# Optimization experiments

Hardware: AMD Instinct MI355X
Metric: run time of the kernel (lower is better)

## Reference

```python
import jax, jax.numpy as jnp
import numpy as np

B = 2048   # batch
C = 64     # EEG channels (num_eegch)
T = 125    # time samples -> pool5 -> 25 -> (p=5, 5)
H = 8      # num_heads
L = 6      # num_layers
D = 16     # num_projected_features
QK = 8     # qkv_len
P = 5      # tokens before cls
EPS = 1e-5


def setup_inputs() -> dict:
    key = jax.random.key(0)
    ks = iter(jax.random.split(key, 64))

    def nrm(shape, s=0.05):
        return jax.random.normal(next(ks), shape, jnp.float32) * s

    return {
        "x": jax.random.normal(next(ks), (B, 1, C, T), jnp.float32),
        "conv_t_w": nrm((8, 1, 1, 63)),
        "conv_t_b": nrm((8,)),
        "bn1_g": 1.0 + nrm((8,)),
        "bn1_b": nrm((8,)),
        "bn1_m": nrm((8,)),
        "bn1_v": 1.0 + 0.1 * jax.random.uniform(next(ks), (8,), jnp.float32),
        "conv_s_w": nrm((16, 1, C, 1)),
        "conv_s_b": nrm((16,)),
        "bn2_g": 1.0 + nrm((16,)),
        "bn2_b": nrm((16,)),
        "bn2_m": nrm((16,)),
        "bn2_v": 1.0 + 0.1 * jax.random.uniform(next(ks), (16,), jnp.float32),
        "proj_w": nrm((D, 16 * 5)),
        "proj_b": nrm((D,)),
        "cls_token": nrm((1, 1, D), 1.0),
        "pe": nrm((1, P + 1, D), 1.0),
        "qkv_w": nrm((L, 3 * H * QK, D)),
        "qkv_b": nrm((L, 3 * H * QK)),
        "out_w": nrm((L, D, H * QK)),
        "out_b": nrm((L, D)),
        "ln1_g": jnp.ones((L, D), jnp.float32),
        "ln1_b": jnp.zeros((L, D), jnp.float32),
        "ln2_g": jnp.ones((L, D), jnp.float32),
        "ln2_b": jnp.zeros((L, D), jnp.float32),
        "mlp_w1": nrm((L, 2 * D, D)),
        "mlp_b1": nrm((L, 2 * D)),
        "mlp_w2": nrm((L, D, 2 * D)),
        "mlp_b2": nrm((L, D)),
        "head_ln_g": jnp.ones((D,), jnp.float32),
        "head_ln_b": jnp.zeros((D,), jnp.float32),
        "head_w": nrm((2, D)),
        "head_b": nrm((2,)),
    }


def _bn(z, g, b, m, v):
    s = (g * jax.lax.rsqrt(v + EPS))[None, :, None, None]
    return (z - m[None, :, None, None]) * s + b[None, :, None, None]


def _ln(z, g, b):
    m = z.mean(-1, keepdims=True)
    var = jnp.mean((z - m) ** 2, -1, keepdims=True)
    return (z - m) * jax.lax.rsqrt(var + EPS) * g + b


def _forward(x, conv_t_w, conv_t_b, bn1_g, bn1_b, bn1_m, bn1_v,
             conv_s_w, conv_s_b, bn2_g, bn2_b, bn2_m, bn2_v,
             proj_w, proj_b, cls_token, pe,
             qkv_w, qkv_b, out_w, out_b, ln1_g, ln1_b, ln2_g, ln2_b,
             mlp_w1, mlp_b1, mlp_w2, mlp_b2,
             head_ln_g, head_ln_b, head_w, head_b):
    b = x.shape[0]
    dn = ('NCHW', 'OIHW', 'NCHW')
    # temporal conv, 'same' padding on width (kernel 63 -> pad 31/31)
    y = jax.lax.conv_general_dilated(x, conv_t_w, (1, 1), [(0, 0), (31, 31)], dimension_numbers=dn)
    y = _bn(y + conv_t_b[None, :, None, None], bn1_g, bn1_b, bn1_m, bn1_v)
    # grouped spatial conv collapses the EEG-channel axis
    y = jax.lax.conv_general_dilated(y, conv_s_w, (1, 1), 'VALID', dimension_numbers=dn, feature_group_count=8)
    y = _bn(y + conv_s_b[None, :, None, None], bn2_g, bn2_b, bn2_m, bn2_v)
    y = jax.nn.elu(y)                              # (b,16,1,125)
    y = y.reshape(b, 16, 1, T // 5, 5).mean(-1)    # avg_pool2d (1,5) -> (b,16,1,25)
    # dropout: identity at inference
    y = y.reshape(b, 16, 1, P, 5)
    y = jnp.swapaxes(y, 3, 4)
    tok = jnp.swapaxes(y.reshape(b, 16 * 5, P), 1, 2)   # (b,5,80)
    tok = tok @ proj_w.T + proj_b                       # (b,5,16)
    z = jnp.concatenate([jnp.broadcast_to(cls_token, (b, 1, D)), tok], axis=1) + pe  # (b,6,16)
    scale = QK ** -0.5
    for i in range(L):
        h1 = _ln(z, ln1_g[i], ln1_b[i])
        qkv = h1 @ qkv_w[i].T + qkv_b[i]                # (b,6,3*H*QK)
        q, k, v = jnp.split(qkv, 3, axis=-1)
        q = q.reshape(b, P + 1, H, QK).transpose(0, 2, 1, 3)
        k = k.reshape(b, P + 1, H, QK).transpose(0, 2, 1, 3)
        v = v.reshape(b, P + 1, H, QK).transpose(0, 2, 1, 3)
        att = jax.nn.softmax(jnp.einsum('bhsd,bhtd->bhst', q, k) * scale, axis=-1)
        o = jnp.einsum('bhst,bhtd->bhsd', att, v).transpose(0, 2, 1, 3).reshape(b, P + 1, H * QK)
        z = o @ out_w[i].T + out_b[i] + z
        h2 = _ln(z, ln2_g[i], ln2_b[i])
        m = jax.nn.gelu(h2 @ mlp_w1[i].T + mlp_b1[i], approximate=False) @ mlp_w2[i].T + mlp_b2[i]
        z = m + z
    cls = _ln(z[:, 0, :], head_ln_g, head_ln_b)
    return jax.nn.softmax(cls @ head_w.T + head_b, axis=-1)


def reference(x, conv_t_w, conv_t_b, bn1_g, bn1_b, bn1_m, bn1_v,
              conv_s_w, conv_s_b, bn2_g, bn2_b, bn2_m, bn2_v,
              proj_w, proj_b, cls_token, pe,
              qkv_w, qkv_b, out_w, out_b, ln1_g, ln1_b, ln2_g, ln2_b,
              mlp_w1, mlp_b1, mlp_w2, mlp_b2,
              head_ln_g, head_ln_b, head_w, head_b):
    return _forward(x, conv_t_w, conv_t_b, bn1_g, bn1_b, bn1_m, bn1_v,
                    conv_s_w, conv_s_b, bn2_g, bn2_b, bn2_m, bn2_v,
                    proj_w, proj_b, cls_token, pe,
                    qkv_w, qkv_b, out_w, out_b, ln1_g, ln1_b, ln2_g, ln2_b,
                    mlp_w1, mlp_b1, mlp_w2, mlp_b2,
                    head_ln_g, head_ln_b, head_w, head_b)
```

## Files before the change

kernel.cpp:

```cpp
#include <hip/hip_runtime.h>

#define WAVE_SYNC() do { asm volatile("" ::: "memory"); \
                         __builtin_amdgcn_wave_barrier(); \
                         asm volatile("" ::: "memory"); } while (0)

typedef _Float16 h2 __attribute__((ext_vector_type(2)));
typedef _Float16 h4 __attribute__((ext_vector_type(4)));
typedef _Float16 h8 __attribute__((ext_vector_type(8)));

__device__ __forceinline__ float fdot2(h2 a, h2 b, float c) {
#if defined(__has_builtin)
#if __has_builtin(__builtin_amdgcn_fdot2)
    return __builtin_amdgcn_fdot2(a, b, c, false);
#else
    return (float)a[0]*(float)b[0] + (float)a[1]*(float)b[1] + c;
#endif
#else
    return (float)a[0]*(float)b[0] + (float)a[1]*(float)b[1] + c;
#endif
}

__device__ __forceinline__ float dot8h(h8 a, h8 b, float c) {
    float s = c;
    #pragma unroll
    for (int i = 0; i < 4; ++i) {
        h2 x = {a[2*i], a[2*i+1]};
        h2 y = {b[2*i], b[2*i+1]};
        s = fdot2(x, y, s);
    }
    return s;
}

__device__ __forceinline__ float dot16h(h8 a0, h8 a1, h8 b0, h8 b1, float c) {
    return dot8h(a1, b1, dot8h(a0, b0, c));
}

__device__ __forceinline__ float ln_norm16(float z, float g, float bb) {
    float s = z, q = z * z;
    #pragma unroll
    for (int off = 8; off >= 1; off >>= 1) {
        s += __shfl_xor(s, off, 16);
        q += __shfl_xor(q, off, 16);
    }
    float mean = s * 0.0625f;
    float var  = q * 0.0625f - mean * mean;
    return (z - mean) * rsqrtf(var + 1e-5f) * g + bb;
}

__device__ __forceinline__ float gelu_exact(float a) {
    float xa = fabsf(a) * 0.70710678118654752f;
    float tt = 1.f / (1.f + 0.3275911f * xa);
    float poly = tt * (0.254829592f + tt * (-0.284496736f + tt * (1.421413741f
               + tt * (-1.453152027f + tt * 1.061405429f))));
    float erfv = 1.f - poly * __expf(-xa * xa);
    erfv = a >= 0.f ? erfv : -erfv;
    return 0.5f * a * (1.f + erfv);
}


#define F_XSTR 204
#define F_PL   4000
#define TOKF   4704
#define FUSED_TOTF 4784

#define WQKVH 0
#define WOUTH 4608
#define WM1H  5760
#define WM2H  6528
#define BQKVF 3584
#define BOUTF 3776
#define BM1F  3792
#define BM2F  3824
#define LN1GF 3840
#define LN1BF 3856
#define LN2GF 3872
#define LN2BF 3888
#define SCR0  7808
#define SH1H  0
#define SQKVH 144
#define SMHSH 1344

extern "C" __global__ __launch_bounds__(128, 2)
void eegnet_fused(
    const float* __restrict__ x,
    const float* __restrict__ conv_t_w, const float* __restrict__ conv_t_b,
    const float* __restrict__ bn1_g, const float* __restrict__ bn1_b,
    const float* __restrict__ bn1_m, const float* __restrict__ bn1_v,
    const float* __restrict__ conv_s_w, const float* __restrict__ conv_s_b,
    const float* __restrict__ bn2_g, const float* __restrict__ bn2_b,
    const float* __restrict__ bn2_m, const float* __restrict__ bn2_v,
    const float* __restrict__ proj_w, const float* __restrict__ proj_b,
    const float* __restrict__ cls_token, const float* __restrict__ pe,
    const float* __restrict__ qkv_w, const float* __restrict__ qkv_b,
    const float* __restrict__ out_w, const float* __restrict__ out_b,
    const float* __restrict__ ln1_g, const float* __restrict__ ln1_b,
    const float* __restrict__ ln2_g, const float* __restrict__ ln2_b,
    const float* __restrict__ mlp_w1, const float* __restrict__ mlp_b1,
    const float* __restrict__ mlp_w2, const float* __restrict__ mlp_b2,
    const float* __restrict__ head_ln_g, const float* __restrict__ head_ln_b,
    const float* __restrict__ head_w, const float* __restrict__ head_b,
    float* __restrict__ out)
{
    __shared__ __align__(16) float sm[FUSED_TOTF];
    _Float16* smh = reinterpret_cast<_Float16*>(sm);
    _Float16* xr  = reinterpret_cast<_Float16*>(sm);

    const int tid = threadIdx.x;
    const int b   = blockIdx.x;

    {
        const float4* xb4 = reinterpret_cast<const float4*>(x + (size_t)b * 8000);
        #pragma unroll
        for (int k = 0; k < 16; ++k) {
            int g = min(tid + k * 128, 1999);
            float4 v = xb4[g];
            h4 hv = {(_Float16)v.x, (_Float16)v.y, (_Float16)v.z, (_Float16)v.w};
            *reinterpret_cast<h4*>(&xr[4 * g]) = hv;
        }
    }
    __syncthreads();

    float acc[16];
    #pragma unroll
    for (int o = 0; o < 16; ++o) acc[o] = 0.f;
    {
        const int t = min(tid, 124);
        #pragma unroll 8
        for (int c = 0; c < 64; ++c) {
            float xv = (float)xr[c * 125 + t];
            #pragma unroll
            for (int o = 0; o < 16; ++o)
                acc[o] += conv_s_w[o * 64 + c] * xv;
        }
    }
    __syncthreads();

    for (int i = tid; i < 16 * 79; i += 128) {
        int row = i / 79, k = i - row * 79;
        int off = (k < 32) ? k : (k + 125);
        sm[row * F_XSTR + off] = 0.f;
    }
    if (tid < 125) {
        #pragma unroll
        for (int o = 0; o < 16; ++o)
            sm[o * F_XSTR + 32 + tid] = acc[o];
    }
    __syncthreads();

    const int oo = tid & 15, qg8 = tid >> 4, gg = oo >> 1;
    {
        float sa, cc;
        {
            float s1 = bn1_g[gg] * rsqrtf(bn1_v[gg] + 1e-5f);
            float b1 = (conv_t_b[gg] - bn1_m[gg]) * s1 + bn1_b[gg];
            float s2 = bn2_g[oo] * rsqrtf(bn2_v[oo] + 1e-5f);
            float ssum = 0.f;
            const float4* csw = reinterpret_cast<const float4*>(conv_s_w + oo * 64);
            #pragma unroll
            for (int i = 0; i < 16; ++i) {
                float4 v = csw[i];
                ssum += v.x + v.y + v.z + v.w;
            }
            sa = s1 * s2;
            cc = (b1 * ssum + conv_s_b[oo] - bn2_m[oo]) * s2 + bn2_b[oo];
        }
        float wt[63];
        #pragma unroll
        for (int k = 0; k < 63; ++k) wt[k] = conv_t_w[gg * 63 + k];

        #pragma unroll 2
        for (int jj = 0; jj < 4; ++jj) {
            int j  = qg8 * 4 + jj;
            int jc = min(j, 24);
            int base = oo * F_XSTR + 5 * jc + 1;
            float acc5[5] = {0.f, 0.f, 0.f, 0.f, 0.f};
            #pragma unroll
            for (int m = 0; m < 67; ++m) {
                float xv = sm[base + m];
                #pragma unroll
                for (int u = 0; u < 5; ++u)
                    if (u <= m && m - u <= 62) acc5[u] += wt[m - u] * xv;
            }
            float psum = 0.f;
            #pragma unroll
            for (int u = 0; u < 5; ++u) {
                float v = acc5[u] * sa + cc;
                psum += (v > 0.f) ? v : (__expf(v) - 1.f);
            }
            if (j == jc) sm[F_PL + oo * 28 + j] = psum * 0.2f;
        }
    }
    __syncthreads();

    if (tid < 80) {
        int p = tid >> 4, dd = tid & 15;
        float acc3 = proj_b[dd];
        const float4* wp = reinterpret_cast<const float4*>(proj_w + dd * 80);
        #pragma unroll
        for (int i = 0; i < 20; ++i) {
            float4 w4 = wp[i];
            acc3 += w4.x * sm[F_PL + ((4*i+0)/5) * 28 + p * 5 + ((4*i+0)%5)];
            acc3 += w4.y * sm[F_PL + ((4*i+1)/5) * 28 + p * 5 + ((4*i+1)%5)];
            acc3 += w4.z * sm[F_PL + ((4*i+2)/5) * 28 + p * 5 + ((4*i+2)%5)];
            acc3 += w4.w * sm[F_PL + ((4*i+3)/5) * 28 + p * 5 + ((4*i+3)%5)];
        }
        sm[TOKF + p * 16 + dd] = acc3;
    }
    __syncthreads();

    const int d16 = tid & 15, qg = tid >> 4;
    const int t6c = min(qg, 5);
    const int wav = tid >> 6, al = tid & 63;
    const int sb  = SCR0;
    const int sA  = blockIdx.x;

    float zA;
    {
        float peV = pe[t6c * 16 + d16];
        if (t6c == 0) zA = cls_token[d16] + peV;
        else          zA = sm[TOKF + (t6c - 1) * 16 + d16] + peV;
    }

    #pragma unroll 1
    for (int li = 0; li < 6; ++li) {
        __syncthreads();

        {
            const float4* s1 = reinterpret_cast<const float4*>(qkv_w + li * 3072);
            #pragma unroll
            for (int it = 0; it < 6; ++it) {
                int i = tid + it * 128;
                float4 v = s1[i];
                int j = i >> 2, k = (i & 3) << 2;
                h4 hv = {(_Float16)v.x, (_Float16)v.y, (_Float16)v.z, (_Float16)v.w};
                *reinterpret_cast<h4*>(&smh[WQKVH + j * 24 + k]) = hv;
            }
            const float4* s2 = reinterpret_cast<const float4*>(out_w + li * 1024);
            #pragma unroll
            for (int it = 0; it < 2; ++it) {
                int i = tid + it * 128;
                float4 v = s2[i];
                int j = i >> 4, k = (i & 15) << 2;
                h4 hv = {(_Float16)v.x, (_Float16)v.y, (_Float16)v.z, (_Float16)v.w};
                *reinterpret_cast<h4*>(&smh[WOUTH + j * 72 + k]) = hv;
            }
            {
                float4 v = reinterpret_cast<const float4*>(mlp_w1 + li * 512)[tid];
                int j = tid >> 2, k = (tid & 3) << 2;
                h4 hv = {(_Float16)v.x, (_Float16)v.y, (_Float16)v.z, (_Float16)v.w};
                *reinterpret_cast<h4*>(&smh[WM1H + j * 24 + k]) = hv;
            }
            {
                float4 v = reinterpret_cast<const float4*>(mlp_w2 + li * 512)[tid];
                int j = tid >> 3, k = (tid & 7) << 2;
                h4 hv = {(_Float16)v.x, (_Float16)v.y, (_Float16)v.z, (_Float16)v.w};
                *reinterpret_cast<h4*>(&smh[WM2H + j * 40 + k]) = hv;
            }
            #pragma unroll
            for (int p = 0; p < 2; ++p) {
                int i = tid + p * 128;
                if (i < 192)       sm[BQKVF + i]       = qkv_b[li * 192 + i];
                else if (i < 208)  sm[BOUTF + i - 192] = out_b[li * 16 + i - 192];
                else if (i < 240)  sm[BM1F + i - 208]  = mlp_b1[li * 32 + i - 208];
                else               sm[BM2F + i - 240]  = mlp_b2[li * 16 + i - 240];
            }
            if (tid >= 64 && tid < 80)        sm[LN1GF + tid - 64]  = ln1_g[li * 16 + tid - 64];
            else if (tid >= 80 && tid < 96)   sm[LN1BF + tid - 80]  = ln1_b[li * 16 + tid - 80];
            else if (tid >= 96 && tid < 112)  sm[LN2GF + tid - 96]  = ln2_g[li * 16 + tid - 96];
            else if (tid >= 112 && tid < 128) sm[LN2BF + tid - 112] = ln2_b[li * 16 + tid - 112];
        }
        __syncthreads();

        {
            float g = sm[LN1GF + d16], bb = sm[LN1BF + d16];
            smh[sb + SH1H + t6c * 24 + d16] = (_Float16)ln_norm16(zA, g, bb);
        }
        WAVE_SYNC();

        h8 hA0 = *reinterpret_cast<const h8*>(&smh[sb + SH1H + t6c * 24]);
        h8 hA1 = *reinterpret_cast<const h8*>(&smh[sb + SH1H + t6c * 24 + 8]);

        #pragma unroll 2
        for (int r = 0; r < 12; ++r) {
            int j = d16 + 16 * r;
            h8 w0 = *reinterpret_cast<const h8*>(&smh[WQKVH + j * 24]);
            h8 w1 = *reinterpret_cast<const h8*>(&smh[WQKVH + j * 24 + 8]);
            float bb = sm[BQKVF + j];
            smh[sb + SQKVH + t6c * 200 + j] = (_Float16)dot16h(hA0, hA1, w0, w1, bb);
        }
        __syncthreads();

        {
            bool act = (wav == 0) ? (al < 32) : (al < 16);
            if (act) {
                int h  = al & 7;
                int qs = (wav == 0) ? (al >> 3) : 4 + (al >> 3);
                const int qoff = sb + SQKVH + qs * 200 + h * 8;
                h8 qA = *reinterpret_cast<const h8*>(&smh[qoff]);
                float scA[6];
                #pragma unroll
                for (int t = 0; t < 6; ++t) {
                    h8 kA = *reinterpret_cast<const h8*>(&smh[sb + SQKVH + t * 200 + 64 + h * 8]);
                    scA[t] = dot8h(qA, kA, 0.f) * 0.35355339059327373f;
                }
                float mxA = scA[0];
                #pragma unroll
                for (int t = 1; t < 6; ++t) mxA = fmaxf(mxA, scA[t]);
                float suA = 0.f;
                #pragma unroll
                for (int t = 0; t < 6; ++t) { scA[t] = __expf(scA[t] - mxA); suA += scA[t]; }
                float ivA = 1.f / suA;
                h2 oA[4];
                #pragma unroll
                for (int k2 = 0; k2 < 4; ++k2) oA[k2] = h2{0, 0};
                #pragma unroll
                for (int t = 0; t < 6; ++t) {
                    h8 vA = *reinterpret_cast<const h8*>(&smh[sb + SQKVH + t * 200 + 128 + h * 8]);
                    _Float16 aa = (_Float16)(scA[t] * ivA);
                    h2 av = {aa, aa};
                    #pragma unroll
                    for (int k2 = 0; k2 < 4; ++k2) {
                        h2 va = {vA[2*k2], vA[2*k2+1]};
                        oA[k2] += av * va;
                    }
                }
                h8 stA;
                #pragma unroll
                for (int k2 = 0; k2 < 4; ++k2) {
                    stA[2*k2] = oA[k2][0]; stA[2*k2+1] = oA[k2][1];
                }
                *reinterpret_cast<h8*>(&smh[qoff]) = stA;
            }
        }
        WAVE_SYNC();

        {
            float aA = sm[BOUTF + d16];
            #pragma unroll
            for (int i = 0; i < 8; ++i) {
                h8 wv = *reinterpret_cast<const h8*>(&smh[WOUTH + d16 * 72 + 8 * i]);
                h8 va = *reinterpret_cast<const h8*>(&smh[sb + SQKVH + t6c * 200 + 8 * i]);
                aA = dot8h(va, wv, aA);
            }
            zA += aA;
        }

        {
            float g = sm[LN2GF + d16], bb = sm[LN2BF + d16];
            smh[sb + SH1H + t6c * 24 + d16] = (_Float16)ln_norm16(zA, g, bb);
        }
        WAVE_SYNC();
        hA0 = *reinterpret_cast<const h8*>(&smh[sb + SH1H + t6c * 24]);
        hA1 = *reinterpret_cast<const h8*>(&smh[sb + SH1H + t6c * 24 + 8]);

        #pragma unroll
        for (int r = 0; r < 2; ++r) {
            int uu = d16 + 16 * r;
            h8 w0 = *reinterpret_cast<const h8*>(&smh[WM1H + uu * 24]);
            h8 w1 = *reinterpret_cast<const h8*>(&smh[WM1H + uu * 24 + 8]);
            float bb = sm[BM1F + uu];
            float aA = dot16h(hA0, hA1, w0, w1, bb);
            smh[sb + SMHSH + t6c * 40 + uu] = (_Float16)gelu_exact(aA);
        }
        WAVE_SYNC();

        {
            float aA = sm[BM2F + d16];
            #pragma unroll
            for (int i = 0; i < 4; ++i) {
                h8 wv = *reinterpret_cast<const h8*>(&smh[WM2H + d16 * 40 + 8 * i]);
                h8 va = *reinterpret_cast<const h8*>(&smh[sb + SMHSH + t6c * 40 + 8 * i]);
                aA = dot8h(va, wv, aA);
            }
            zA += aA;
        }
    }

    if (tid < 16) {
        float g = head_ln_g[d16], bb = head_ln_b[d16];
        float w0 = head_w[d16], w1 = head_w[16 + d16];
        float cvA = ln_norm16(zA, g, bb);
        float pA0 = cvA * w0, pA1 = cvA * w1;
        #pragma unroll
        for (int off = 8; off >= 1; off >>= 1) {
            pA0 += __shfl_xor(pA0, off, 16);
            pA1 += __shfl_xor(pA1, off, 16);
        }
        if (tid == 0) {
            float l0 = pA0 + head_b[0], l1 = pA1 + head_b[1];
            float mx = fmaxf(l0, l1);
            float e0 = __expf(l0 - mx), e1 = __expf(l1 - mx);
            float inv = 1.f / (e0 + e1);
            out[sA * 2 + 0] = e0 * inv;
            out[sA * 2 + 1] = e1 * inv;
        }
    }
}

extern "C" void kernel_launch(void* const* d_in, const int* in_sizes, int n_in,
                              void* d_out, int out_size, void* d_ws, size_t ws_size,
                              hipStream_t stream) {
    (void)n_in; (void)ws_size; (void)out_size; (void)d_ws;
    const float* a0  = (const float*)d_in[0];
    const float* a1  = (const float*)d_in[1];
    const float* a2  = (const float*)d_in[2];
    const float* a3  = (const float*)d_in[3];
    const float* a4  = (const float*)d_in[4];
    const float* a5  = (const float*)d_in[5];
    const float* a6  = (const float*)d_in[6];
    const float* a7  = (const float*)d_in[7];
    const float* a8  = (const float*)d_in[8];
    const float* a9  = (const float*)d_in[9];
    const float* a10 = (const float*)d_in[10];
    const float* a11 = (const float*)d_in[11];
    const float* a12 = (const float*)d_in[12];
    const float* a13 = (const float*)d_in[13];
    const float* a14 = (const float*)d_in[14];
    const float* a15 = (const float*)d_in[15];
    const float* a16 = (const float*)d_in[16];
    const float* a17 = (const float*)d_in[17];
    const float* a18 = (const float*)d_in[18];
    const float* a19 = (const float*)d_in[19];
    const float* a20 = (const float*)d_in[20];
    const float* a21 = (const float*)d_in[21];
    const float* a22 = (const float*)d_in[22];
    const float* a23 = (const float*)d_in[23];
    const float* a24 = (const float*)d_in[24];
    const float* a25 = (const float*)d_in[25];
    const float* a26 = (const float*)d_in[26];
    const float* a27 = (const float*)d_in[27];
    const float* a28 = (const float*)d_in[28];
    const float* a29 = (const float*)d_in[29];
    const float* a30 = (const float*)d_in[30];
    const float* a31 = (const float*)d_in[31];
    const float* a32 = (const float*)d_in[32];

    int Bn = in_sizes[0] / (64 * 125);

    eegnet_fused<<<Bn, 128, 0, stream>>>(
        a0, a1, a2, a3, a4, a5, a6, a7, a8, a9, a10, a11, a12,
        a13, a14, a15, a16, a17, a18, a19, a20, a21, a22, a23, a24,
        a25, a26, a27, a28, a29, a30, a31, a32, (float*)d_out);
}
```

Baseline: 252.5 us.

## Process two samples per 256-thread block, sharing per-layer weight staging

Each block now runs two batch samples, one per 128-thread half, so every layer's weights and biases are converted and staged in shared memory once for both samples. The input is streamed in four chunks of 16 channels to keep the per-sample scratch small. The spatial-conv output buffer moves to fp16 with a tighter stride. The intent is to halve weight-staging traffic and barrier overhead per sample. In exchange, block-wide barriers now couple the two samples, launch bounds change to 256 threads with one block per CU hint, and Bn is assumed even.

After: 301.0 us. 19.2% more time.

```diff
diff --git a/kernel.cpp b/kernel.cpp
--- a/kernel.cpp
+++ b/kernel.cpp
@@ -58,10 +58,10 @@
 }
 
 
-#define F_XSTR 204
-#define F_PL   4000
-#define TOKF   4704
-#define FUSED_TOTF 4784
+#define A_WH   5088
+#define A_WF   2544
+#define XSPOH  2048
+#define XSTRH  190
 
 #define WQKVH 0
 #define WOUTH 4608
@@ -76,11 +76,14 @@
 #define LN2GF 3872
 #define LN2BF 3888
 #define SCR0  7808
+#define SSTRH 1584
 #define SH1H  0
 #define SQKVH 144
 #define SMHSH 1344
-
-extern "C" __global__ __launch_bounds__(128, 2)
+#define TOKF  5488
+#define FUSED_TOTF 5648
+
+extern "C" __global__ __launch_bounds__(256, 1)
 void eegnet_fused(
     const float* __restrict__ x,
     const float* __restrict__ conv_t_w, const float* __restrict__ conv_t_b,
@@ -103,53 +106,60 @@
 {
     __shared__ __align__(16) float sm[FUSED_TOTF];
     _Float16* smh = reinterpret_cast<_Float16*>(sm);
-    _Float16* xr  = reinterpret_cast<_Float16*>(sm);
 
     const int tid = threadIdx.x;
-    const int b   = blockIdx.x;
-
-    {
-        const float4* xb4 = reinterpret_cast<const float4*>(x + (size_t)b * 8000);
-        #pragma unroll
-        for (int k = 0; k < 16; ++k) {
-            int g = min(tid + k * 128, 1999);
-            float4 v = xb4[g];
-            h4 hv = {(_Float16)v.x, (_Float16)v.y, (_Float16)v.z, (_Float16)v.w};
-            *reinterpret_cast<h4*>(&xr[4 * g]) = hv;
-        }
-    }
-    __syncthreads();
+    const int w   = tid >> 7;
+    const int l   = tid & 127;
+    const int b   = blockIdx.x * 2 + w;
+
+    _Float16* rg  = smh + w * A_WH;
+    _Float16* xsp = smh + w * A_WH + XSPOH;
+    float*    pool = sm + w * A_WF;
+
+    for (int i = l; i < 1040; i += 128) {
+        int row = i / 65, k = i - row * 65;
+        int off = (k < 32) ? k : (k + 125);
+        xsp[row * XSTRH + off] = (_Float16)0.f;
+    }
 
     float acc[16];
     #pragma unroll
     for (int o = 0; o < 16; ++o) acc[o] = 0.f;
     {
-        const int t = min(tid, 124);
-        #pragma unroll 8
-        for (int c = 0; c < 64; ++c) {
-            float xv = (float)xr[c * 125 + t];
-            #pragma unroll
-            for (int o = 0; o < 16; ++o)
-                acc[o] += conv_s_w[o * 64 + c] * xv;
-        }
+        const float4* xb4 = reinterpret_cast<const float4*>(x + (size_t)b * 8000);
+        const int t = min(l, 124);
+        #pragma unroll
+        for (int cc = 0; cc < 4; ++cc) {
+            #pragma unroll
+            for (int k = 0; k < 4; ++k) {
+                int g = min(k * 128 + l, 499);
+                float4 v = xb4[cc * 500 + g];
+                h4 hv = {(_Float16)v.x, (_Float16)v.y, (_Float16)v.z, (_Float16)v.w};
+                *reinterpret_cast<h4*>(&rg[4 * g]) = hv;
+            }
+            __syncthreads();
+            #pragma unroll
+            for (int cl = 0; cl < 16; ++cl) {
+                float xv = (float)rg[cl * 125 + t];
+                int c = cc * 16 + cl;
+                #pragma unroll
+                for (int o = 0; o < 16; ++o)
+                    acc[o] += conv_s_w[o * 64 + c] * xv;
+            }
+            __syncthreads();
+        }
+    }
+
+    if (l < 125) {
+        #pragma unroll
+        for (int o = 0; o < 16; ++o)
+            xsp[o * XSTRH + 32 + l] = (_Float16)acc[o];
     }
     __syncthreads();
 
-    for (int i = tid; i < 16 * 79; i += 128) {
-        int row = i / 79, k = i - row * 79;
-        int off = (k < 32) ? k : (k + 125);
-        sm[row * F_XSTR + off] = 0.f;
-    }
-    if (tid < 125) {
-        #pragma unroll
-        for (int o = 0; o < 16; ++o)
-            sm[o * F_XSTR + 32 + tid] = acc[o];
-    }
-    __syncthreads();
-
-    const int oo = tid & 15, qg8 = tid >> 4, gg = oo >> 1;
     {
-        float sa, cc;
+        const int oo = l & 15, qg8 = l >> 4, gg = oo >> 1;
+        float sa, cc2;
         {
             float s1 = bn1_g[gg] * rsqrtf(bn1_v[gg] + 1e-5f);
             float b1 = (conv_t_b[gg] - bn1_m[gg]) * s1 + bn1_b[gg];
@@ -162,7 +172,7 @@
                 ssum += v.x + v.y + v.z + v.w;
             }
             sa = s1 * s2;
-            cc = (b1 * ssum + conv_s_b[oo] - bn2_m[oo]) * s2 + bn2_b[oo];
+            cc2 = (b1 * ssum + conv_s_b[oo] - bn2_m[oo]) * s2 + bn2_b[oo];
         }
         float wt[63];
         #pragma unroll
@@ -172,11 +182,11 @@
         for (int jj = 0; jj < 4; ++jj) {
             int j  = qg8 * 4 + jj;
             int jc = min(j, 24);
-            int base = oo * F_XSTR + 5 * jc + 1;
+            int base = oo * XSTRH + 5 * jc + 1;
             float acc5[5] = {0.f, 0.f, 0.f, 0.f, 0.f};
             #pragma unroll
             for (int m = 0; m < 67; ++m) {
-                float xv = sm[base + m];
+                float xv = (float)xsp[base + m];
                 #pragma unroll
                 for (int u = 0; u < 5; ++u)
                     if (u <= m && m - u <= 62) acc5[u] += wt[m - u] * xv;
@@ -184,41 +194,43 @@
             float psum = 0.f;
             #pragma unroll
             for (int u = 0; u < 5; ++u) {
-                float v = acc5[u] * sa + cc;
+                float v = acc5[u] * sa + cc2;
                 psum += (v > 0.f) ? v : (__expf(v) - 1.f);
             }
-            if (j == jc) sm[F_PL + oo * 28 + j] = psum * 0.2f;
+            if (j == jc) pool[oo * 28 + j] = psum * 0.2f;
         }
     }
     __syncthreads();
 
-    if (tid < 80) {
-        int p = tid >> 4, dd = tid & 15;
+    if (l < 80) {
+        int p = l >> 4, dd = l & 15;
         float acc3 = proj_b[dd];
         const float4* wp = reinterpret_cast<const float4*>(proj_w + dd * 80);
         #pragma unroll
         for (int i = 0; i < 20; ++i) {
             float4 w4 = wp[i];
-            acc3 += w4.x * sm[F_PL + ((4*i+0)/5) * 28 + p * 5 + ((4*i+0)%5)];
-            acc3 += w4.y * sm[F_PL + ((4*i+1)/5) * 28 + p * 5 + ((4*i+1)%5)];
-            acc3 += w4.z * sm[F_PL + ((4*i+2)/5) * 28 + p * 5 + ((4*i+2)%5)];
-            acc3 += w4.w * sm[F_PL + ((4*i+3)/5) * 28 + p * 5 + ((4*i+3)%5)];
-        }
-        sm[TOKF + p * 16 + dd] = acc3;
+            acc3 += w4.x * pool[((4*i+0)/5) * 28 + p * 5 + ((4*i+0)%5)];
+            acc3 += w4.y * pool[((4*i+1)/5) * 28 + p * 5 + ((4*i+1)%5)];
+            acc3 += w4.z * pool[((4*i+2)/5) * 28 + p * 5 + ((4*i+2)%5)];
+            acc3 += w4.w * pool[((4*i+3)/5) * 28 + p * 5 + ((4*i+3)%5)];
+        }
+        sm[TOKF + w * 80 + p * 16 + dd] = acc3;
     }
     __syncthreads();
 
-    const int d16 = tid & 15, qg = tid >> 4;
+    const int ss  = tid >> 7;
+    const int u   = tid & 127;
+    const int d16 = u & 15, qg = u >> 4;
     const int t6c = min(qg, 5);
-    const int wav = tid >> 6, al = tid & 63;
-    const int sb  = SCR0;
-    const int sA  = blockIdx.x;
+    const int wav = u >> 6, al = u & 63;
+    const int sb  = SCR0 + ss * SSTRH;
+    const int sA  = blockIdx.x * 2;
 
     float zA;
     {
         float peV = pe[t6c * 16 + d16];
         if (t6c == 0) zA = cls_token[d16] + peV;
-        else          zA = sm[TOKF + (t6c - 1) * 16 + d16] + peV;
+        else          zA = sm[TOKF + ss * 80 + (t6c - 1) * 16 + d16] + peV;
     }
 
     #pragma unroll 1
@@ -228,42 +240,35 @@
         {
             const float4* s1 = reinterpret_cast<const float4*>(qkv_w + li * 3072);
             #pragma unroll
-            for (int it = 0; it < 6; ++it) {
-                int i = tid + it * 128;
+            for (int it = 0; it < 3; ++it) {
+                int i = tid + it * 256;
                 float4 v = s1[i];
                 int j = i >> 2, k = (i & 3) << 2;
                 h4 hv = {(_Float16)v.x, (_Float16)v.y, (_Float16)v.z, (_Float16)v.w};
                 *reinterpret_cast<h4*>(&smh[WQKVH + j * 24 + k]) = hv;
             }
-            const float4* s2 = reinterpret_cast<const float4*>(out_w + li * 1024);
-            #pragma unroll
-            for (int it = 0; it < 2; ++it) {
-                int i = tid + it * 128;
-                float4 v = s2[i];
-                int j = i >> 4, k = (i & 15) << 2;
+            {
+                float4 v = reinterpret_cast<const float4*>(out_w + li * 1024)[tid];
+                int j = tid >> 4, k = (tid & 15) << 2;
                 h4 hv = {(_Float16)v.x, (_Float16)v.y, (_Float16)v.z, (_Float16)v.w};
                 *reinterpret_cast<h4*>(&smh[WOUTH + j * 72 + k]) = hv;
             }
-            {
+            if (tid < 128) {
                 float4 v = reinterpret_cast<const float4*>(mlp_w1 + li * 512)[tid];
                 int j = tid >> 2, k = (tid & 3) << 2;
                 h4 hv = {(_Float16)v.x, (_Float16)v.y, (_Float16)v.z, (_Float16)v.w};
                 *reinterpret_cast<h4*>(&smh[WM1H + j * 24 + k]) = hv;
-            }
-            {
-                float4 v = reinterpret_cast<const float4*>(mlp_w2 + li * 512)[tid];
-                int j = tid >> 3, k = (tid & 7) << 2;
+            } else {
+                int i = tid - 128;
+                float4 v = reinterpret_cast<const float4*>(mlp_w2 + li * 512)[i];
+                int j = i >> 3, k = (i & 7) << 2;
                 h4 hv = {(_Float16)v.x, (_Float16)v.y, (_Float16)v.z, (_Float16)v.w};
                 *reinterpret_cast<h4*>(&smh[WM2H + j * 40 + k]) = hv;
             }
-            #pragma unroll
-            for (int p = 0; p < 2; ++p) {
-                int i = tid + p * 128;
-                if (i < 192)       sm[BQKVF + i]       = qkv_b[li * 192 + i];
-                else if (i < 208)  sm[BOUTF + i - 192] = out_b[li * 16 + i - 192];
-                else if (i < 240)  sm[BM1F + i - 208]  = mlp_b1[li * 32 + i - 208];
-                else               sm[BM2F + i - 240]  = mlp_b2[li * 16 + i - 240];
-            }
+            if (tid < 192) sm[BQKVF + tid] = qkv_b[li * 192 + tid];
+            else if (tid < 208) sm[BOUTF + tid - 192] = out_b[li * 16 + tid - 192];
+            else if (tid < 240) sm[BM1F + tid - 208]  = mlp_b1[li * 32 + tid - 208];
+            else               sm[BM2F + tid - 240]  = mlp_b2[li * 16 + tid - 240];
             if (tid >= 64 && tid < 80)        sm[LN1GF + tid - 64]  = ln1_g[li * 16 + tid - 64];
             else if (tid >= 80 && tid < 96)   sm[LN1BF + tid - 80]  = ln1_b[li * 16 + tid - 80];
             else if (tid >= 96 && tid < 112)  sm[LN2GF + tid - 96]  = ln2_g[li * 16 + tid - 96];
@@ -376,7 +381,7 @@
         }
     }
 
-    if (tid < 16) {
+    if (u < 16) {
         float g = head_ln_g[d16], bb = head_ln_b[d16];
         float w0 = head_w[d16], w1 = head_w[16 + d16];
         float cvA = ln_norm16(zA, g, bb);
@@ -386,13 +391,13 @@
             pA0 += __shfl_xor(pA0, off, 16);
             pA1 += __shfl_xor(pA1, off, 16);
         }
-        if (tid == 0) {
+        if (u == 0) {
             float l0 = pA0 + head_b[0], l1 = pA1 + head_b[1];
             float mx = fmaxf(l0, l1);
             float e0 = __expf(l0 - mx), e1 = __expf(l1 - mx);
             float inv = 1.f / (e0 + e1);
-            out[sA * 2 + 0] = e0 * inv;
-            out[sA * 2 + 1] = e1 * inv;
+            out[(sA + ss) * 2 + 0] = e0 * inv;
+            out[(sA + ss) * 2 + 1] = e1 * inv;
         }
     }
 }
@@ -437,7 +442,7 @@
 
     int Bn = in_sizes[0] / (64 * 125);
 
-    eegnet_fused<<<Bn, 128, 0, stream>>>(
+    eegnet_fused<<<Bn / 2, 256, 0, stream>>>(
         a0, a1, a2, a3, a4, a5, a6, a7, a8, a9, a10, a11, a12,
         a13, a14, a15, a16, a17, a18, a19, a20, a21, a22, a23, a24,
         a25, a26, a27, a28, a29, a30, a31, a32, (float*)d_out);
```
